# Kernel tuning notes

Hardware: AMD Instinct MI355X
Metric: run time of the kernel (lower is better)

## Reference

```python
import jax, jax.numpy as jnp
import numpy as np

NEG_SLOPE = 0.2
LN_EPS = 1e-5


def gat_conv(x, edge_index, W, att_src, att_dst, bias, heads, out_ch, concat):
    """PyG-style GATConv with add_self_loops=True, eval mode (no dropout)."""
    N = x.shape[0]
    loop = jnp.arange(N, dtype=edge_index.dtype)
    src = jnp.concatenate([edge_index[0], loop])
    dst = jnp.concatenate([edge_index[1], loop])
    h = (x @ W).reshape(N, heads, out_ch)                      # [N,H,C]
    a_src = jnp.sum(h * att_src, axis=-1)                      # [N,H]
    a_dst = jnp.sum(h * att_dst, axis=-1)                      # [N,H]
    e = jax.nn.leaky_relu(a_src[src] + a_dst[dst], NEG_SLOPE)  # [E,H]
    emax = jax.ops.segment_max(e, dst, num_segments=N)         # [N,H]
    ex = jnp.exp(e - emax[dst])
    denom = jax.ops.segment_sum(ex, dst, num_segments=N)       # [N,H]
    alpha = ex / denom[dst]                                    # [E,H]
    msg = h[src] * alpha[..., None]                            # [E,H,C]
    out = jax.ops.segment_sum(msg, dst, num_segments=N)        # [N,H,C]
    out = out.reshape(N, heads * out_ch) if concat else out.mean(axis=1)
    return out + bias


def layer_norm(x, w, b):
    mu = x.mean(-1, keepdims=True)
    var = jnp.mean((x - mu) ** 2, -1, keepdims=True)
    return (x - mu) * jax.lax.rsqrt(var + LN_EPS) * w + b


def setup_inputs() -> dict:
    key = jax.random.key(0)
    ks = jax.random.split(key, 16)
    N, E, R = 50000, 800000, 16
    node_dim, res_dim, hidden, heads = 128, 64, 64, 2
    s = lambda fan: 1.0 / np.sqrt(fan)
    return {
        "x": jax.random.normal(ks[0], (N, node_dim), jnp.float32),
        "edge_index": jax.random.randint(ks[1], (2, E), 0, N, jnp.int64),
        "resource_features": jax.random.normal(ks[2], (N, R, res_dim), jnp.float32),
        "W1": jax.random.normal(ks[3], (node_dim, heads * hidden), jnp.float32) * s(node_dim),
        "att_src1": jax.random.normal(ks[4], (heads, hidden), jnp.float32) * s(hidden),
        "att_dst1": jax.random.normal(ks[5], (heads, hidden), jnp.float32) * s(hidden),
        "b1": jnp.zeros((heads * hidden,), jnp.float32),
        "W2": jax.random.normal(ks[6], (heads * hidden, hidden), jnp.float32) * s(heads * hidden),
        "att_src2": jax.random.normal(ks[7], (1, hidden), jnp.float32) * s(hidden),
        "att_dst2": jax.random.normal(ks[8], (1, hidden), jnp.float32) * s(hidden),
        "b2": jnp.zeros((hidden,), jnp.float32),
        "ln_w": jnp.ones((hidden,), jnp.float32),
        "ln_b": jnp.zeros((hidden,), jnp.float32),
        "res_W": jax.random.normal(ks[9], (res_dim, hidden), jnp.float32) * s(res_dim),
        "res_b": jnp.zeros((hidden,), jnp.float32),
    }


def reference(x, edge_index, resource_features, W1, att_src1, att_dst1, b1,
              W2, att_src2, att_dst2, b2, ln_w, ln_b, res_W, res_b):
    hidden = W2.shape[1]
    heads = att_src1.shape[0]
    h = jax.nn.elu(gat_conv(x, edge_index, W1, att_src1, att_dst1, b1,
                            heads, hidden, concat=True))
    h = gat_conv(h, edge_index, W2, att_src2, att_dst2, b2,
                 1, hidden, concat=False)
    h = layer_norm(h, ln_w, ln_b)                              # [N, hidden]
    R = resource_features.shape[1]
    x_expanded = jnp.broadcast_to(h[:, None, :], (h.shape[0], R, hidden))
    res_emb = jax.nn.elu(resource_features @ res_W + res_b)    # [N,R,hidden]
    return jnp.concatenate([x_expanded, res_emb], axis=-1)     # [N,R,2*hidden]
```

## Files before the change

kernel.cpp:

```cpp
#include <hip/hip_runtime.h>
#include <hip/hip_bf16.h>
#include <math.h>

#define LEAKY_SLOPE 0.2f
#define LN_EPS 1e-5f

typedef __attribute__((ext_vector_type(4))) float f32x4;
typedef __attribute__((ext_vector_type(8))) short short8;

__device__ __forceinline__ float leaky_relu(float x) { return x >= 0.f ? x : LEAKY_SLOPE * x; }
__device__ __forceinline__ float elu1(float x) { return x > 0.f ? x : expm1f(x); }
__device__ __forceinline__ short f2bf(float f) {
    union { __hip_bfloat16 b; short s; } u;
    u.b = __float2bfloat16(f);
    return u.s;
}
__device__ __forceinline__ float bflo(unsigned u) { union { unsigned i; float f; } x; x.i = u << 16; return x.f; }
__device__ __forceinline__ float bfhi(unsigned u) { union { unsigned i; float f; } x; x.i = u & 0xffff0000u; return x.f; }
__device__ __forceinline__ float sbf(short s) { union { unsigned i; float f; } x; x.i = ((unsigned)(unsigned short)s) << 16; return x.f; }
__device__ __forceinline__ unsigned fkey(float f) {
    unsigned b = __float_as_uint(f);
    return b ^ (unsigned)(((int)b >> 31) | 0x80000000);
}
__device__ __forceinline__ float funkey(unsigned k) {
    unsigned b = (k & 0x80000000u) ? (k ^ 0x80000000u) : ~k;
    return __uint_as_float(b);
}

#define DETECT_IS64(ei, E)                                              \
    __shared__ int s_is64;                                              \
    {                                                                   \
        if (threadIdx.x < 64) {                                         \
            int v = (threadIdx.x < (E)) ? ((const int*)(ei))[2 * threadIdx.x + 1] : 0; \
            unsigned long long b = __ballot(v != 0);                    \
            if (threadIdx.x == 0) s_is64 = (b == 0ULL);                 \
        }                                                               \
        __syncthreads();                                                \
    }

#define SUBW1 130
#define DEGB 512
__global__ __launch_bounds__(256) void k_fat1(
    const float* __restrict__ x, const float* __restrict__ W1,
    const float* __restrict__ att_s, const float* __restrict__ att_d,
    short* __restrict__ h1, float* __restrict__ a_src, float* __restrict__ a_dst,
    unsigned* __restrict__ amax, int N,
    const void* __restrict__ ei, int E, int* __restrict__ deg,
    const float* __restrict__ resW, short* __restrict__ rwb, int nbG)
{
    if ((int)blockIdx.x >= nbG) {
        const int b0 = (int)blockIdx.x - nbG;
        if (b0 == 0) {
            for (int idx = threadIdx.x; idx < 4096; idx += 256) {
                int f = idx >> 9, lane = (idx >> 3) & 63, j = idx & 7;
                int kk = f >> 2, nc = f & 3;
                int k = kk * 32 + (lane >> 4) * 8 + j;
                int col = nc * 16 + (lane & 15);
                rwb[idx] = f2bf(resW[k * 64 + col]);
            }
        }
        DETECT_IS64(ei, E)
        const int is64 = s_is64;
        for (int e = b0 * 256 + threadIdx.x; e < E; e += DEGB * 256) {
            int d = is64 ? (int)((const long long*)ei)[(size_t)E + e] : ((const int*)ei)[(size_t)E + e];
            atomicAdd(&deg[d], 1);
        }
        return;
    }
    __shared__ short WT[16 * SUBW1 * 8];
    __shared__ float sb[64 * 4];
    __shared__ float wm[8];
    const int t = threadIdx.x;
    const int w = t >> 6, l = t & 63, lr = l & 15, lk = l >> 4;
    const int n0 = blockIdx.x * 64;
    for (int idx = t; idx < 16384; idx += 256) {
        int k = idx >> 7, col = idx & 127;
        WT[((k >> 3) * SUBW1 + col) * 8 + (k & 7)] = f2bf(W1[idx]);
    }
    sb[t] = 0.f;
    __syncthreads();

    f32x4 acc[4][2];
    #pragma unroll
    for (int mt = 0; mt < 4; ++mt)
        #pragma unroll
        for (int nt = 0; nt < 2; ++nt) acc[mt][nt] = (f32x4){0.f, 0.f, 0.f, 0.f};

    #pragma unroll
    for (int ks = 0; ks < 4; ++ks) {
        short8 bfr[2];
        #pragma unroll
        for (int nt = 0; nt < 2; ++nt) {
            int col = w * 32 + nt * 16 + lr;
            int kk = ks * 4 + lk;
            bfr[nt] = *(const short8*)&WT[(kk * SUBW1 + col) * 8];
        }
        #pragma unroll
        for (int mt = 0; mt < 4; ++mt) {
            int row = n0 + mt * 16 + lr; if (row >= N) row = N - 1;
            const float* ap = x + (size_t)row * 128 + ks * 32 + lk * 8;
            float4 u0 = *(const float4*)ap;
            float4 u1 = *(const float4*)(ap + 4);
            short8 af;
            af[0] = f2bf(u0.x); af[1] = f2bf(u0.y); af[2] = f2bf(u0.z); af[3] = f2bf(u0.w);
            af[4] = f2bf(u1.x); af[5] = f2bf(u1.y); af[6] = f2bf(u1.z); af[7] = f2bf(u1.w);
            acc[mt][0] = __builtin_amdgcn_mfma_f32_16x16x32_bf16(af, bfr[0], acc[mt][0], 0, 0, 0);
            acc[mt][1] = __builtin_amdgcn_mfma_f32_16x16x32_bf16(af, bfr[1], acc[mt][1], 0, 0, 0);
        }
    }

    const int head = w >> 1;
    float asv[2], adv[2];
    #pragma unroll
    for (int nt = 0; nt < 2; ++nt) {
        int ci = (w & 1) * 32 + nt * 16 + lr;
        asv[nt] = att_s[head * 64 + ci];
        adv[nt] = att_d[head * 64 + ci];
    }
    #pragma unroll
    for (int mt = 0; mt < 4; ++mt) {
        #pragma unroll
        for (int i = 0; i < 4; ++i) {
            float ps = acc[mt][0][i] * asv[0] + acc[mt][1][i] * asv[1];
            float pd = acc[mt][0][i] * adv[0] + acc[mt][1][i] * adv[1];
            #pragma unroll
            for (int o = 1; o < 16; o <<= 1) { ps += __shfl_xor(ps, o); pd += __shfl_xor(pd, o); }
            int rl = mt * 16 + lk * 4 + i;
            if (lr == 0) {
                atomicAdd(&sb[rl * 4 + head], ps);
                atomicAdd(&sb[rl * 4 + 2 + head], pd);
            }
            int row = n0 + rl;
            if (row < N) {
                h1[(size_t)row * 128 + w * 32 + lr]      = f2bf(acc[mt][0][i]);
                h1[(size_t)row * 128 + w * 32 + 16 + lr] = f2bf(acc[mt][1][i]);
            }
        }
    }
    __syncthreads();
    int nl = t >> 2, q = t & 3, n = n0 + nl;
    float v = sb[t];
    bool ok = (n < N);
    if (ok) {
        if (q == 0) a_src[n * 2 + 0] = v;
        else if (q == 1) a_src[n * 2 + 1] = v;
        else if (q == 2) a_dst[n * 2 + 0] = v;
        else a_dst[n * 2 + 1] = v;
    }
    float m0 = (ok && q == 0) ? v : -1e30f;
    float m1 = (ok && q == 1) ? v : -1e30f;
    #pragma unroll
    for (int o = 32; o; o >>= 1) { m0 = fmaxf(m0, __shfl_xor(m0, o)); m1 = fmaxf(m1, __shfl_xor(m1, o)); }
    if (l == 0) { wm[w] = m0; wm[4 + w] = m1; }
    __syncthreads();
    if (t == 0) {
        float M0 = fmaxf(fmaxf(wm[0], wm[1]), fmaxf(wm[2], wm[3]));
        float M1 = fmaxf(fmaxf(wm[4], wm[5]), fmaxf(wm[6], wm[7]));
        atomicMax(&amax[0], fkey(M0));
        atomicMax(&amax[1], fkey(M1));
    }
}

__global__ __launch_bounds__(256) void k_bsum(const int* __restrict__ deg, int* __restrict__ bsum, int n)
{
    __shared__ int ws[4];
    const int base = blockIdx.x * 1024;
    int s = 0;
    for (int j = threadIdx.x; j < 1024; j += 256) {
        int i = base + j;
        s += (i < n) ? deg[i] : 0;
    }
    #pragma unroll
    for (int o = 32; o; o >>= 1) s += __shfl_down(s, o);
    if ((threadIdx.x & 63) == 0) ws[threadIdx.x >> 6] = s;
    __syncthreads();
    if (threadIdx.x == 0) bsum[blockIdx.x] = ws[0] + ws[1] + ws[2] + ws[3];
}

__global__ __launch_bounds__(1024) void k_scan3(const int* __restrict__ deg, const int* __restrict__ bsum,
                                                int* __restrict__ offs, int* __restrict__ cursor,
                                                int n, int nb)
{
    __shared__ int ws[16];
    __shared__ int bb;
    const int i = blockIdx.x * 1024 + threadIdx.x;
    const int l = threadIdx.x & 63, w = threadIdx.x >> 6;
    if (threadIdx.x < 64) {
        int v = 0;
        for (int b = l; b < (int)blockIdx.x; b += 64) v += (b < nb) ? bsum[b] : 0;
        #pragma unroll
        for (int o = 32; o; o >>= 1) v += __shfl_xor(v, o);
        if (l == 0) bb = v;
    }
    int v = (i < n) ? deg[i] : 0;
    int x = v;
    #pragma unroll
    for (int o = 1; o < 64; o <<= 1) { int y = __shfl_up(x, o); if (l >= o) x += y; }
    if (l == 63) ws[w] = x;
    __syncthreads();
    if (threadIdx.x < 16) {
        int s = ws[threadIdx.x];
        #pragma unroll
        for (int o = 1; o < 16; o <<= 1) { int y = __shfl_up(s, o); if (threadIdx.x >= o) s += y; }
        ws[threadIdx.x] = s;
    }
    __syncthreads();
    int add = (w ? ws[w - 1] : 0) + bb;
    if (i < n) {
        offs[i + 1] = x + add;
        cursor[i] = x + add - v;
    }
    if (blockIdx.x == 0 && threadIdx.x == 0) offs[0] = 0;
}

__global__ __launch_bounds__(256) void k_scatter(const void* __restrict__ ei, int E,
                                                 int* __restrict__ cursor, int* __restrict__ csr_src)
{
    DETECT_IS64(ei, E)
    const int is64 = s_is64;
    for (int e = blockIdx.x * blockDim.x + threadIdx.x; e < E; e += gridDim.x * blockDim.x) {
        int s, d;
        if (is64) {
            const long long* p = (const long long*)ei;
            s = (int)p[e]; d = (int)p[(size_t)E + e];
        } else {
            const int* p = (const int*)ei;
            s = p[e]; d = p[(size_t)E + e];
        }
        int pos = atomicAdd(&cursor[d], 1);
        csr_src[pos] = s;
    }
}

__global__ __launch_bounds__(256) void k_layer1(
    const short* __restrict__ h1, const float* __restrict__ a_s, const float* __restrict__ a_d,
    const int* __restrict__ offs, const int* __restrict__ csr,
    const float* __restrict__ b1, const unsigned* __restrict__ amax,
    short* __restrict__ h1a, int N,
    const float* __restrict__ res, const short* __restrict__ rwb,
    const float* __restrict__ resb, float* __restrict__ out)
{
    const int w = threadIdx.x >> 6, l = threadIdx.x & 63;
    const int n = blockIdx.x * 4 + w;
    if (n >= N) return;
    const float2 adp = *(const float2*)&a_d[2 * n];
    const float2 asp = *(const float2*)&a_s[2 * n];
    const float C0 = leaky_relu(funkey(amax[0]) + adp.x);
    const float C1 = leaky_relu(funkey(amax[1]) + adp.y);
    const float es0 = leaky_relu(asp.x + adp.x) - C0;
    const float es1 = leaky_relu(asp.y + adp.y) - C1;
    const int hsel = l >> 5;
    const int o0 = offs[n], o1 = offs[n + 1];

    float den0 = 0.f, den1 = 0.f;
    float cl0 = 0.f, ch0 = 0.f, cl1 = 0.f, ch1 = 0.f;
    float cl2 = 0.f, ch2 = 0.f, cl3 = 0.f, ch3 = 0.f;
    for (int base = o0; base < o1; base += 64) {
        const int cnt = min(64, o1 - base);
        int sidx = 0; float p0 = 0.f, p1 = 0.f;
        if (l < cnt) {
            sidx = csr[base + l];
            float2 av = *(const float2*)&a_s[2 * sidx];
            p0 = __expf(leaky_relu(av.x + adp.x) - C0);
            p1 = __expf(leaky_relu(av.y + adp.y) - C1);
        }
        den0 += p0; den1 += p1;
        int j = 0;
        for (; j + 4 <= cnt; j += 4) {
            int s0 = __shfl(sidx, j),     s1 = __shfl(sidx, j + 1);
            int s2 = __shfl(sidx, j + 2), s3 = __shfl(sidx, j + 3);
            float q00 = __shfl(p0, j),     q10 = __shfl(p1, j);
            float q01 = __shfl(p0, j + 1), q11 = __shfl(p1, j + 1);
            float q02 = __shfl(p0, j + 2), q12 = __shfl(p1, j + 2);
            float q03 = __shfl(p0, j + 3), q13 = __shfl(p1, j + 3);
            unsigned u0 = *(const unsigned*)(h1 + (size_t)s0 * 128 + 2 * l);
            unsigned u1 = *(const unsigned*)(h1 + (size_t)s1 * 128 + 2 * l);
            unsigned u2 = *(const unsigned*)(h1 + (size_t)s2 * 128 + 2 * l);
            unsigned u3 = *(const unsigned*)(h1 + (size_t)s3 * 128 + 2 * l);
            float w0 = hsel ? q10 : q00, w1 = hsel ? q11 : q01;
            float w2 = hsel ? q12 : q02, w3 = hsel ? q13 : q03;
            cl0 += w0 * bflo(u0); ch0 += w0 * bfhi(u0);
            cl1 += w1 * bflo(u1); ch1 += w1 * bfhi(u1);
            cl2 += w2 * bflo(u2); ch2 += w2 * bfhi(u2);
            cl3 += w3 * bflo(u3); ch3 += w3 * bfhi(u3);
        }
        for (; j < cnt; ++j) {
            int sa = __shfl(sidx, j);
            float qa0 = __shfl(p0, j), qa1 = __shfl(p1, j);
            unsigned ua = *(const unsigned*)(h1 + (size_t)sa * 128 + 2 * l);
            float wa = hsel ? qa1 : qa0;
            cl0 += wa * bflo(ua); ch0 += wa * bfhi(ua);
        }
    }
    #pragma unroll
    for (int o = 32; o; o >>= 1) { den0 += __shfl_xor(den0, o); den1 += __shfl_xor(den1, o); }
    const float psf0 = __expf(es0), psf1 = __expf(es1);
    const float inv0 = 1.f / (den0 + psf0), inv1 = 1.f / (den1 + psf1);

    unsigned us = *(const unsigned*)(h1 + (size_t)n * 128 + 2 * l);
    const float psf = hsel ? psf1 : psf0;
    float acc0 = cl0 + cl1 + cl2 + cl3 + psf * bflo(us);
    float acc1 = ch0 + ch1 + ch2 + ch3 + psf * bfhi(us);
    const float invh = hsel ? inv1 : inv0;
    float2 bv = *(const float2*)&b1[2 * l];
    float v0 = elu1(acc0 * invh + bv.x);
    float v1 = elu1(acc1 * invh + bv.y);
    unsigned up = ((unsigned)(unsigned short)f2bf(v0)) | (((unsigned)(unsigned short)f2bf(v1)) << 16);
    *(unsigned*)(h1a + (size_t)n * 128 + 2 * l) = up;

    __builtin_amdgcn_sched_barrier(0);
    {
        const int lr = l & 15, lk = l >> 4;
        const float* rp = res + (size_t)n * 1024 + lr * 64 + lk * 8;
        const f32x4 f0 = __builtin_nontemporal_load((const f32x4*)(rp));
        const f32x4 f1 = __builtin_nontemporal_load((const f32x4*)(rp + 4));
        const f32x4 f2 = __builtin_nontemporal_load((const f32x4*)(rp + 32));
        const f32x4 f3 = __builtin_nontemporal_load((const f32x4*)(rp + 36));
        short8 fa0, fa1;
        fa0[0] = f2bf(f0[0]); fa0[1] = f2bf(f0[1]); fa0[2] = f2bf(f0[2]); fa0[3] = f2bf(f0[3]);
        fa0[4] = f2bf(f1[0]); fa0[5] = f2bf(f1[1]); fa0[6] = f2bf(f1[2]); fa0[7] = f2bf(f1[3]);
        fa1[0] = f2bf(f2[0]); fa1[1] = f2bf(f2[1]); fa1[2] = f2bf(f2[2]); fa1[3] = f2bf(f2[3]);
        fa1[4] = f2bf(f3[0]); fa1[5] = f2bf(f3[1]); fa1[6] = f2bf(f3[2]); fa1[7] = f2bf(f3[3]);
        const short8* rw8 = (const short8*)rwb;
        float* ob = out + (size_t)n * 2048;
        #pragma unroll
        for (int nc = 0; nc < 4; ++nc) {
            f32x4 a = (f32x4){0.f, 0.f, 0.f, 0.f};
            a = __builtin_amdgcn_mfma_f32_16x16x32_bf16(fa0, rw8[nc * 64 + l], a, 0, 0, 0);
            a = __builtin_amdgcn_mfma_f32_16x16x32_bf16(fa1, rw8[(4 + nc) * 64 + l], a, 0, 0, 0);
            const float rb = resb[nc * 16 + lr];
            #pragma unroll
            for (int ii = 0; ii < 4; ++ii)
                __builtin_nontemporal_store(elu1(a[ii] + rb), ob + (lk * 4 + ii) * 128 + 64 + nc * 16 + lr);
        }
    }
}

#define SUBW2 66
__global__ __launch_bounds__(256) void k_gemm2m(
    const short* __restrict__ h1a, const float* __restrict__ W2,
    const float* __restrict__ att_s, const float* __restrict__ att_d,
    short* __restrict__ h2, float* __restrict__ a_src, float* __restrict__ a_dst,
    unsigned* __restrict__ amax, int N)
{
    __shared__ short WT[16 * SUBW2 * 8];
    __shared__ float sb[64 * 2];
    __shared__ float wm[4];
    const int t = threadIdx.x;
    const int w = t >> 6, l = t & 63, lr = l & 15, lk = l >> 4;
    const int n0 = blockIdx.x * 64;
    for (int idx = t; idx < 8192; idx += 256) {
        int k = idx >> 6, col = idx & 63;
        WT[((k >> 3) * SUBW2 + col) * 8 + (k & 7)] = f2bf(W2[idx]);
    }
    if (t < 128) sb[t] = 0.f;
    __syncthreads();

    f32x4 acc[4];
    #pragma unroll
    for (int mt = 0; mt < 4; ++mt) acc[mt] = (f32x4){0.f, 0.f, 0.f, 0.f};

    #pragma unroll
    for (int ks = 0; ks < 4; ++ks) {
        short8 bfr = *(const short8*)&WT[((ks * 4 + lk) * SUBW2 + w * 16 + lr) * 8];
        #pragma unroll
        for (int mt = 0; mt < 4; ++mt) {
            int row = n0 + mt * 16 + lr; if (row >= N) row = N - 1;
            short8 af = *(const short8*)(h1a + (size_t)row * 128 + ks * 32 + lk * 8);
            acc[mt] = __builtin_amdgcn_mfma_f32_16x16x32_bf16(af, bfr, acc[mt], 0, 0, 0);
        }
    }

    const float asv = att_s[w * 16 + lr], adv = att_d[w * 16 + lr];
    #pragma unroll
    for (int mt = 0; mt < 4; ++mt) {
        #pragma unroll
        for (int i = 0; i < 4; ++i) {
            float ps = acc[mt][i] * asv;
            float pd = acc[mt][i] * adv;
            #pragma unroll
            for (int o = 1; o < 16; o <<= 1) { ps += __shfl_xor(ps, o); pd += __shfl_xor(pd, o); }
            int rl = mt * 16 + lk * 4 + i;
            if (lr == 0) {
                atomicAdd(&sb[rl * 2 + 0], ps);
                atomicAdd(&sb[rl * 2 + 1], pd);
            }
            int row = n0 + rl;
            if (row < N) h2[(size_t)row * 64 + w * 16 + lr] = f2bf(acc[mt][i]);
        }
    }
    __syncthreads();
    float v = (t < 128) ? sb[t] : -1e30f;
    int n = n0 + (t >> 1);
    bool ok = (t < 128) && (n < N);
    if (ok) {
        if (t & 1) a_dst[n] = v;
        else       a_src[n] = v;
    }
    float m0 = (ok && !(t & 1)) ? v : -1e30f;
    #pragma unroll
    for (int o = 32; o; o >>= 1) m0 = fmaxf(m0, __shfl_xor(m0, o));
    if (l == 0) wm[w] = m0;
    __syncthreads();
    if (t == 0) {
        float M0 = fmaxf(fmaxf(wm[0], wm[1]), fmaxf(wm[2], wm[3]));
        atomicMax(&amax[0], fkey(M0));
    }
}

__global__ __launch_bounds__(256) void k_tail(
    const short* __restrict__ h2, const float* __restrict__ a_s, const float* __restrict__ a_d,
    const int* __restrict__ offs, const int* __restrict__ csr,
    const float* __restrict__ b2, const float* __restrict__ lnw, const float* __restrict__ lnb,
    const unsigned* __restrict__ amax, float* __restrict__ out, int N)
{
    const int w = threadIdx.x >> 6, l = threadIdx.x & 63;
    const int lr = l & 15, lk = l >> 4;
    const int n = blockIdx.x * 4 + w;
    if (n >= N) return;
    const float b2l = b2[l], lnwl = lnw[l], lnbl = lnb[l];
    const float Am = funkey(amax[0]);

    const float adv = a_d[n];
    const float C = leaky_relu(Am + adv);
    const float es = leaky_relu(a_s[n] + adv) - C;
    const int o0 = offs[n], o1 = offs[n + 1];
    float den = 0.f, a0 = 0.f, a1 = 0.f, a2 = 0.f, a3 = 0.f;
    for (int base = o0; base < o1; base += 64) {
        const int cnt = min(64, o1 - base);
        int sidx = 0; float pv = 0.f;
        if (l < cnt) {
            sidx = csr[base + l];
            pv = __expf(leaky_relu(a_s[sidx] + adv) - C);
        }
        den += pv;
        int j = 0;
        for (; j + 4 <= cnt; j += 4) {
            int s0 = __shfl(sidx, j),     s1 = __shfl(sidx, j + 1);
            int s2 = __shfl(sidx, j + 2), s3 = __shfl(sidx, j + 3);
            float q0 = __shfl(pv, j),     q1 = __shfl(pv, j + 1);
            float q2 = __shfl(pv, j + 2), q3 = __shfl(pv, j + 3);
            a0 += q0 * sbf(h2[(size_t)s0 * 64 + l]);
            a1 += q1 * sbf(h2[(size_t)s1 * 64 + l]);
            a2 += q2 * sbf(h2[(size_t)s2 * 64 + l]);
            a3 += q3 * sbf(h2[(size_t)s3 * 64 + l]);
        }
        for (; j < cnt; ++j) {
            int sa = __shfl(sidx, j);
            float qa = __shfl(pv, j);
            a0 += qa * sbf(h2[(size_t)sa * 64 + l]);
        }
    }
    #pragma unroll
    for (int o = 32; o; o >>= 1) den += __shfl_xor(den, o);
    const float psf = __expf(es);
    const float inv = 1.f / (den + psf);
    float o = (a0 + a1 + a2 + a3 + psf * sbf(h2[(size_t)n * 64 + l])) * inv + b2l;
    float mu = o;
    #pragma unroll
    for (int off = 32; off; off >>= 1) mu += __shfl_xor(mu, off);
    mu *= (1.f / 64.f);
    float d = o - mu;
    float vv = d * d;
    #pragma unroll
    for (int off = 32; off; off >>= 1) vv += __shfl_xor(vv, off);
    vv *= (1.f / 64.f);
    const float hl = d * rsqrtf(vv + LN_EPS) * lnwl + lnbl;
    f32x4 hv;
    #pragma unroll
    for (int j = 0; j < 4; ++j) hv[j] = __shfl(hl, lr * 4 + j);
    float* ob = out + (size_t)n * 2048;
    #pragma unroll
    for (int ii = 0; ii < 4; ++ii)
        __builtin_nontemporal_store(hv, (f32x4*)(ob + (lk + 4 * ii) * 128 + lr * 4));
}

extern "C" void kernel_launch(void* const* d_in, const int* in_sizes, int n_in,
                              void* d_out, int out_size, void* d_ws, size_t ws_size,
                              hipStream_t stream)
{
    const float* x   = (const float*)d_in[0];
    const void*  ei  = d_in[1];
    const float* res = (const float*)d_in[2];
    const float* W1  = (const float*)d_in[3];
    const float* as1 = (const float*)d_in[4];
    const float* ad1 = (const float*)d_in[5];
    const float* b1  = (const float*)d_in[6];
    const float* W2  = (const float*)d_in[7];
    const float* as2 = (const float*)d_in[8];
    const float* ad2 = (const float*)d_in[9];
    const float* b2  = (const float*)d_in[10];
    const float* lnw = (const float*)d_in[11];
    const float* lnb = (const float*)d_in[12];
    const float* rW  = (const float*)d_in[13];
    const float* rb  = (const float*)d_in[14];
    float* out = (float*)d_out;

    const int N = in_sizes[0] / 128;
    const int E = in_sizes[1] / 2;
    const int nb = (N + 1023) / 1024;
    const int nbG = (N + 63) / 64;

    char* base = (char*)d_ws;
    size_t off = 0;
    auto alloc = [&](size_t bytes) -> void* {
        void* p = base + off;
        off = (off + bytes + 255) & ~(size_t)255;
        return p;
    };
    short* h1    = (short*)alloc((size_t)N * 128 * 2);
    short* h1a   = (short*)alloc((size_t)N * 128 * 2);
    short* h2    = (short*)alloc((size_t)N * 64 * 2);
    float* a_s1  = (float*)alloc((size_t)N * 2 * 4);
    float* a_d1  = (float*)alloc((size_t)N * 2 * 4);
    float* a_s2  = (float*)alloc((size_t)N * 4);
    float* a_d2  = (float*)alloc((size_t)N * 4);
    int* deg     = (int*)alloc((size_t)(N + 8) * 4);
    int* offs    = (int*)alloc((size_t)(N + 1) * 4);
    int* cursor  = (int*)alloc((size_t)N * 4);
    int* csr_src = (int*)alloc((size_t)E * 4);
    int* bsum    = (int*)alloc((size_t)nb * 4);
    short* rwb   = (short*)alloc(4096 * 2);
    unsigned* amax1 = (unsigned*)(deg + N);
    unsigned* amax2 = (unsigned*)(deg + N + 2);

    (void)hipMemsetAsync(deg, 0, (size_t)(N + 8) * 4, stream);
    k_fat1<<<nbG + DEGB, 256, 0, stream>>>(x, W1, as1, ad1, h1, a_s1, a_d1, amax1, N,
                                           ei, E, deg, rW, rwb, nbG);
    k_bsum<<<nb, 256, 0, stream>>>(deg, bsum, N);
    k_scan3<<<nb, 1024, 0, stream>>>(deg, bsum, offs, cursor, N, nb);
    k_scatter<<<512, 256, 0, stream>>>(ei, E, cursor, csr_src);
    k_layer1<<<(N + 3) / 4, 256, 0, stream>>>(h1, a_s1, a_d1, offs, csr_src, b1, amax1, h1a, N,
                                              res, rwb, rb, out);
    k_gemm2m<<<(N + 63) / 64, 256, 0, stream>>>(h1a, W2, as2, ad2, h2, a_s2, a_d2, amax2, N);
    k_tail<<<(N + 3) / 4, 256, 0, stream>>>(h2, a_s2, a_d2, offs, csr_src, b2, lnw, lnb,
                                            amax2, out, N);
}
```

Measured before the change: 335.6 us.

## Pre-gather source attention scores into CSR order and merge scan kernels

The scatter kernel now writes each edge's source attention scores (a_s1) in CSR order, and a new kernel builds a CSR-ordered a_s2 array before the tail. The layer1 and tail kernels then read these scores contiguously instead of gathering them by source index. The separate block-sum kernel is removed, and each scan block instead sums all preceding degrees itself. The residual-feature loads and self-row loads are also hoisted earlier to overlap with the aggregation. This adds an extra kernel launch, about 9.6 MB of extra writes plus reads, and redundant prefix reads in the scan.

```diff
diff --git a/kernel.cpp b/kernel.cpp
--- a/kernel.cpp
+++ b/kernel.cpp
@@ -161,37 +161,20 @@
     }
 }
 
-__global__ __launch_bounds__(256) void k_bsum(const int* __restrict__ deg, int* __restrict__ bsum, int n)
-{
-    __shared__ int ws[4];
-    const int base = blockIdx.x * 1024;
-    int s = 0;
-    for (int j = threadIdx.x; j < 1024; j += 256) {
-        int i = base + j;
-        s += (i < n) ? deg[i] : 0;
-    }
-    #pragma unroll
-    for (int o = 32; o; o >>= 1) s += __shfl_down(s, o);
-    if ((threadIdx.x & 63) == 0) ws[threadIdx.x >> 6] = s;
-    __syncthreads();
-    if (threadIdx.x == 0) bsum[blockIdx.x] = ws[0] + ws[1] + ws[2] + ws[3];
-}
-
-__global__ __launch_bounds__(1024) void k_scan3(const int* __restrict__ deg, const int* __restrict__ bsum,
-                                                int* __restrict__ offs, int* __restrict__ cursor,
-                                                int n, int nb)
+__global__ __launch_bounds__(1024) void k_scan3(const int* __restrict__ deg,
+                                                int* __restrict__ offs, int* __restrict__ cursor, int n)
 {
     __shared__ int ws[16];
+    __shared__ int red[16];
     __shared__ int bb;
     const int i = blockIdx.x * 1024 + threadIdx.x;
     const int l = threadIdx.x & 63, w = threadIdx.x >> 6;
-    if (threadIdx.x < 64) {
-        int v = 0;
-        for (int b = l; b < (int)blockIdx.x; b += 64) v += (b < nb) ? bsum[b] : 0;
-        #pragma unroll
-        for (int o = 32; o; o >>= 1) v += __shfl_xor(v, o);
-        if (l == 0) bb = v;
-    }
+    int pre = 0;
+    const int limit = (int)blockIdx.x * 1024;
+    for (int idx = threadIdx.x; idx < limit; idx += 1024) pre += deg[idx];
+    #pragma unroll
+    for (int o = 32; o; o >>= 1) pre += __shfl_xor(pre, o);
+    if (l == 0) red[w] = pre;
     int v = (i < n) ? deg[i] : 0;
     int x = v;
     #pragma unroll
@@ -203,6 +186,10 @@
         #pragma unroll
         for (int o = 1; o < 16; o <<= 1) { int y = __shfl_up(s, o); if (threadIdx.x >= o) s += y; }
         ws[threadIdx.x] = s;
+        int r = red[threadIdx.x];
+        #pragma unroll
+        for (int o = 8; o; o >>= 1) r += __shfl_xor(r, o, 16);
+        if (threadIdx.x == 0) bb = r;
     }
     __syncthreads();
     int add = (w ? ws[w - 1] : 0) + bb;
@@ -214,7 +201,8 @@
 }
 
 __global__ __launch_bounds__(256) void k_scatter(const void* __restrict__ ei, int E,
-                                                 int* __restrict__ cursor, int* __restrict__ csr_src)
+                                                 int* __restrict__ cursor, int* __restrict__ csr_src,
+                                                 const float* __restrict__ a_s1, float2* __restrict__ csr_as)
 {
     DETECT_IS64(ei, E)
     const int is64 = s_is64;
@@ -229,12 +217,21 @@
         }
         int pos = atomicAdd(&cursor[d], 1);
         csr_src[pos] = s;
-    }
+        csr_as[pos] = *(const float2*)&a_s1[2 * s];
+    }
+}
+
+__global__ __launch_bounds__(256) void k_as2scat(const int* __restrict__ csr_src,
+                                                 const float* __restrict__ a_s2,
+                                                 float* __restrict__ csr_as2, int E)
+{
+    for (int e = blockIdx.x * blockDim.x + threadIdx.x; e < E; e += gridDim.x * blockDim.x)
+        csr_as2[e] = a_s2[csr_src[e]];
 }
 
 __global__ __launch_bounds__(256) void k_layer1(
     const short* __restrict__ h1, const float* __restrict__ a_s, const float* __restrict__ a_d,
-    const int* __restrict__ offs, const int* __restrict__ csr,
+    const int* __restrict__ offs, const int* __restrict__ csr, const float2* __restrict__ csr_as,
     const float* __restrict__ b1, const unsigned* __restrict__ amax,
     short* __restrict__ h1a, int N,
     const float* __restrict__ res, const short* __restrict__ rwb,
@@ -243,6 +240,14 @@
     const int w = threadIdx.x >> 6, l = threadIdx.x & 63;
     const int n = blockIdx.x * 4 + w;
     if (n >= N) return;
+    const int lr = l & 15, lk = l >> 4;
+    const float* rp = res + (size_t)n * 1024 + lr * 64 + lk * 8;
+    const f32x4 f0 = __builtin_nontemporal_load((const f32x4*)(rp));
+    const f32x4 f1 = __builtin_nontemporal_load((const f32x4*)(rp + 4));
+    const f32x4 f2 = __builtin_nontemporal_load((const f32x4*)(rp + 32));
+    const f32x4 f3 = __builtin_nontemporal_load((const f32x4*)(rp + 36));
+    const unsigned us = *(const unsigned*)(h1 + (size_t)n * 128 + 2 * l);
+
     const float2 adp = *(const float2*)&a_d[2 * n];
     const float2 asp = *(const float2*)&a_s[2 * n];
     const float C0 = leaky_relu(funkey(amax[0]) + adp.x);
@@ -260,7 +265,7 @@
         int sidx = 0; float p0 = 0.f, p1 = 0.f;
         if (l < cnt) {
             sidx = csr[base + l];
-            float2 av = *(const float2*)&a_s[2 * sidx];
+            float2 av = csr_as[base + l];
             p0 = __expf(leaky_relu(av.x + adp.x) - C0);
             p1 = __expf(leaky_relu(av.y + adp.y) - C1);
         }
@@ -297,7 +302,6 @@
     const float psf0 = __expf(es0), psf1 = __expf(es1);
     const float inv0 = 1.f / (den0 + psf0), inv1 = 1.f / (den1 + psf1);
 
-    unsigned us = *(const unsigned*)(h1 + (size_t)n * 128 + 2 * l);
     const float psf = hsel ? psf1 : psf0;
     float acc0 = cl0 + cl1 + cl2 + cl3 + psf * bflo(us);
     float acc1 = ch0 + ch1 + ch2 + ch3 + psf * bfhi(us);
@@ -310,12 +314,6 @@
 
     __builtin_amdgcn_sched_barrier(0);
     {
-        const int lr = l & 15, lk = l >> 4;
-        const float* rp = res + (size_t)n * 1024 + lr * 64 + lk * 8;
-        const f32x4 f0 = __builtin_nontemporal_load((const f32x4*)(rp));
-        const f32x4 f1 = __builtin_nontemporal_load((const f32x4*)(rp + 4));
-        const f32x4 f2 = __builtin_nontemporal_load((const f32x4*)(rp + 32));
-        const f32x4 f3 = __builtin_nontemporal_load((const f32x4*)(rp + 36));
         short8 fa0, fa1;
         fa0[0] = f2bf(f0[0]); fa0[1] = f2bf(f0[1]); fa0[2] = f2bf(f0[2]); fa0[3] = f2bf(f0[3]);
         fa0[4] = f2bf(f1[0]); fa0[5] = f2bf(f1[1]); fa0[6] = f2bf(f1[2]); fa0[7] = f2bf(f1[3]);
@@ -410,7 +408,7 @@
 
 __global__ __launch_bounds__(256) void k_tail(
     const short* __restrict__ h2, const float* __restrict__ a_s, const float* __restrict__ a_d,
-    const int* __restrict__ offs, const int* __restrict__ csr,
+    const int* __restrict__ offs, const int* __restrict__ csr, const float* __restrict__ csr_as2,
     const float* __restrict__ b2, const float* __restrict__ lnw, const float* __restrict__ lnb,
     const unsigned* __restrict__ amax, float* __restrict__ out, int N)
 {
@@ -418,6 +416,7 @@
     const int lr = l & 15, lk = l >> 4;
     const int n = blockIdx.x * 4 + w;
     if (n >= N) return;
+    const float selfh = sbf(h2[(size_t)n * 64 + l]);
     const float b2l = b2[l], lnwl = lnw[l], lnbl = lnb[l];
     const float Am = funkey(amax[0]);
 
@@ -431,7 +430,7 @@
         int sidx = 0; float pv = 0.f;
         if (l < cnt) {
             sidx = csr[base + l];
-            pv = __expf(leaky_relu(a_s[sidx] + adv) - C);
+            pv = __expf(leaky_relu(csr_as2[base + l] + adv) - C);
         }
         den += pv;
         int j = 0;
@@ -455,7 +454,7 @@
     for (int o = 32; o; o >>= 1) den += __shfl_xor(den, o);
     const float psf = __expf(es);
     const float inv = 1.f / (den + psf);
-    float o = (a0 + a1 + a2 + a3 + psf * sbf(h2[(size_t)n * 64 + l])) * inv + b2l;
+    float o = (a0 + a1 + a2 + a3 + psf * selfh) * inv + b2l;
     float mu = o;
     #pragma unroll
     for (int off = 32; off; off >>= 1) mu += __shfl_xor(mu, off);
@@ -508,31 +507,32 @@
         off = (off + bytes + 255) & ~(size_t)255;
         return p;
     };
-    short* h1    = (short*)alloc((size_t)N * 128 * 2);
-    short* h1a   = (short*)alloc((size_t)N * 128 * 2);
-    short* h2    = (short*)alloc((size_t)N * 64 * 2);
-    float* a_s1  = (float*)alloc((size_t)N * 2 * 4);
-    float* a_d1  = (float*)alloc((size_t)N * 2 * 4);
-    float* a_s2  = (float*)alloc((size_t)N * 4);
-    float* a_d2  = (float*)alloc((size_t)N * 4);
-    int* deg     = (int*)alloc((size_t)(N + 8) * 4);
-    int* offs    = (int*)alloc((size_t)(N + 1) * 4);
-    int* cursor  = (int*)alloc((size_t)N * 4);
-    int* csr_src = (int*)alloc((size_t)E * 4);
-    int* bsum    = (int*)alloc((size_t)nb * 4);
-    short* rwb   = (short*)alloc(4096 * 2);
+    short* h1     = (short*)alloc((size_t)N * 128 * 2);
+    short* h1a    = (short*)alloc((size_t)N * 128 * 2);
+    short* h2     = (short*)alloc((size_t)N * 64 * 2);
+    float* a_s1   = (float*)alloc((size_t)N * 2 * 4);
+    float* a_d1   = (float*)alloc((size_t)N * 2 * 4);
+    float* a_s2   = (float*)alloc((size_t)N * 4);
+    float* a_d2   = (float*)alloc((size_t)N * 4);
+    int* deg      = (int*)alloc((size_t)(N + 8) * 4);
+    int* offs     = (int*)alloc((size_t)(N + 1) * 4);
+    int* cursor   = (int*)alloc((size_t)N * 4);
+    int* csr_src  = (int*)alloc((size_t)E * 4);
+    float2* csr_as  = (float2*)alloc((size_t)E * 8);
+    float* csr_as2  = (float*)alloc((size_t)E * 4);
+    short* rwb    = (short*)alloc(4096 * 2);
     unsigned* amax1 = (unsigned*)(deg + N);
     unsigned* amax2 = (unsigned*)(deg + N + 2);
 
     (void)hipMemsetAsync(deg, 0, (size_t)(N + 8) * 4, stream);
     k_fat1<<<nbG + DEGB, 256, 0, stream>>>(x, W1, as1, ad1, h1, a_s1, a_d1, amax1, N,
                                            ei, E, deg, rW, rwb, nbG);
-    k_bsum<<<nb, 256, 0, stream>>>(deg, bsum, N);
-    k_scan3<<<nb, 1024, 0, stream>>>(deg, bsum, offs, cursor, N, nb);
-    k_scatter<<<512, 256, 0, stream>>>(ei, E, cursor, csr_src);
-    k_layer1<<<(N + 3) / 4, 256, 0, stream>>>(h1, a_s1, a_d1, offs, csr_src, b1, amax1, h1a, N,
+    k_scan3<<<nb, 1024, 0, stream>>>(deg, offs, cursor, N);
+    k_scatter<<<512, 256, 0, stream>>>(ei, E, cursor, csr_src, a_s1, csr_as);
+    k_layer1<<<(N + 3) / 4, 256, 0, stream>>>(h1, a_s1, a_d1, offs, csr_src, csr_as, b1, amax1, h1a, N,
                                               res, rwb, rb, out);
     k_gemm2m<<<(N + 63) / 64, 256, 0, stream>>>(h1a, W2, as2, ad2, h2, a_s2, a_d2, amax2, N);
-    k_tail<<<(N + 3) / 4, 256, 0, stream>>>(h2, a_s2, a_d2, offs, csr_src, b2, lnw, lnb,
+    k_as2scat<<<512, 256, 0, stream>>>(csr_src, a_s2, csr_as2, E);
+    k_tail<<<(N + 3) / 4, 256, 0, stream>>>(h2, a_s2, a_d2, offs, csr_src, csr_as2, b2, lnw, lnb,
                                             amax2, out, N);
 }
```

Result: slower. 344.8 us (+2.7%).
